# Kernel optimization log

Measured on AMD Instinct MI355X. Metric: run time of the kernel, lower is better.

Reference implementation:

```python
import jax, jax.numpy as jnp
import numpy as np

NUM_IN_CH = 64
DIM = 256
HEADS = 8


def conv1x1(x, w):
    # x: [b,c,h,w], w: [o,c,1,1] -> [b,o,h,w]
    return jnp.einsum('bchw,oc->bohw', x, w[:, :, 0, 0])


def dwconv3(x, w):
    # depthwise 3x3, padding=1; w: [c,1,3,3]
    return jax.lax.conv_general_dilated(
        x, w, window_strides=(1, 1), padding='SAME',
        feature_group_count=x.shape[1],
        dimension_numbers=('NCHW', 'OIHW', 'NCHW'))


def setup_inputs() -> dict:
    key = jax.random.key(0)
    ks = jax.random.split(key, 12)
    B, C, H, W = 8, NUM_IN_CH, 128, 128
    s = 0.02
    return {
        'x': jax.random.normal(ks[0], (B, C, H, W), jnp.float32),
        'y': jax.random.normal(ks[1], (B, C, H, W), jnp.float32),
        'z': jax.random.normal(ks[2], (B, C, H, W), jnp.float32),
        'Wq': jax.random.normal(ks[3], (DIM, C, 1, 1), jnp.float32) * s,
        'Wq_dw': jax.random.normal(ks[4], (DIM, 1, 3, 3), jnp.float32) * s,
        'Wk': jax.random.normal(ks[5], (DIM, C, 1, 1), jnp.float32) * s,
        'Wk_dw': jax.random.normal(ks[6], (DIM, 1, 3, 3), jnp.float32) * s,
        'Wv': jax.random.normal(ks[7], (DIM, C, 1, 1), jnp.float32) * s,
        'Wv_dw': jax.random.normal(ks[8], (DIM, 1, 3, 3), jnp.float32) * s,
        'Wproj': jax.random.normal(ks[9], (DIM, DIM, 1, 1), jnp.float32) * s,
        'Wfus': jax.random.normal(ks[10], (DIM, 3 * C, 1, 1), jnp.float32) * s,
        'temperature': jnp.ones((HEADS, 1, 1), jnp.float32),
    }


def reference(x, y, z, Wq, Wq_dw, Wk, Wk_dw, Wv, Wv_dw, Wproj, Wfus, temperature):
    b, c, h, w = x.shape
    hw = h * w
    q = dwconv3(conv1x1(x, Wq), Wq_dw)
    k = dwconv3(conv1x1(y, Wk), Wk_dw)
    v = dwconv3(conv1x1(z, Wv), Wv_dw)
    f = conv1x1(jnp.concatenate([x, y, z], axis=1), Wfus)

    def to_heads(t):  # [b, dim, h, w] -> [b, head, c_head, hw]
        return t.reshape(b, HEADS, DIM // HEADS, hw)

    q, k, v = to_heads(q), to_heads(k), to_heads(v)
    # L2-normalize over the spatial (hw) axis, eps matches torch F.normalize
    qn = q / jnp.maximum(jnp.sqrt(jnp.sum(q * q, axis=-1, keepdims=True)), 1e-12)
    kn = k / jnp.maximum(jnp.sqrt(jnp.sum(k * k, axis=-1, keepdims=True)), 1e-12)
    attn = jnp.einsum('bhcn,bhdn->bhcd', qn, kn) * temperature  # [b,head,c,c]
    attn = jax.nn.softmax(attn, axis=-1)
    out = jnp.einsum('bhcd,bhdn->bhcn', attn, v).reshape(b, DIM, h, w)
    out = conv1x1(out, Wproj)
    return out + f
```

## Files before the change

### kernel.cpp

```cpp
#include <hip/hip_runtime.h>
#include <cstdint>

#define B_   8
#define CIN  64
#define DIM_ 256
#define H_   128
#define W_   128
#define HW_  (H_*W_)

typedef unsigned short u16;
typedef unsigned int   u32;
typedef short short8 __attribute__((ext_vector_type(8)));
typedef float f32x4  __attribute__((ext_vector_type(4)));

__device__ __forceinline__ u16 f2bf(float f) {
    u32 u = __float_as_uint(f);
    u32 r = (u + 0x7fffu + ((u >> 16) & 1u)) >> 16;
    return (u16)r;
}
__device__ __forceinline__ float bf2f(u16 h) {
    return __uint_as_float(((u32)h) << 16);
}

__global__ __launch_bounds__(512) void convdw_kernel(
    const float* __restrict__ in, const float* __restrict__ Wc,
    const float* __restrict__ Wd, u16* __restrict__ dst)
{
    __shared__ u16 Wt[256 * 64];
    __shared__ u16 Xt[336 * 64];
    __shared__ u16 Pt[64 * 340];
    __shared__ float wlds[9 * 68];

    const int tid = threadIdx.x;
    const int tile = blockIdx.x;
    const int b = blockIdx.y;
    const int y0 = (tile >> 3) * 16;
    const int x0 = (tile & 7) * 16;

    {
        const int row = tid >> 1, hh = tid & 1;
        const float* wp = Wc + (size_t)row * 64 + hh * 32;
        #pragma unroll
        for (int s = 0; s < 4; ++s) {
            float4 f0 = *(const float4*)(wp + s * 8);
            float4 f1 = *(const float4*)(wp + s * 8 + 4);
            uint4 pk;
            pk.x = f2bf(f0.x) | ((u32)f2bf(f0.y) << 16);
            pk.y = f2bf(f0.z) | ((u32)f2bf(f0.w) << 16);
            pk.z = f2bf(f1.x) | ((u32)f2bf(f1.y) << 16);
            pk.w = f2bf(f1.z) | ((u32)f2bf(f1.w) << 16);
            int o = hh * 32 + s * 8;
            *(uint4*)&Wt[row * 64 + (o ^ ((row & 7) << 3))] = pk;
        }
    }
    {
        const float* inb = in + (size_t)b * CIN * HW_;
        for (int i = tid; i < 2592; i += 512) {
            int chg = i / 324;
            int px = i - chg * 324;
            int py = px / 18;
            int pxi = px - py * 18;
            int gy = y0 - 1 + py, gx = x0 - 1 + pxi;
            uint4 pk = make_uint4(0, 0, 0, 0);
            if (gy >= 0 && gy < H_ && gx >= 0 && gx < W_) {
                const float* sp = inb + (size_t)(chg * 8) * HW_ + (size_t)gy * W_ + gx;
                u32 wv[4];
                #pragma unroll
                for (int j = 0; j < 4; ++j) {
                    float a = sp[(size_t)(2 * j) * HW_];
                    float c = sp[(size_t)(2 * j + 1) * HW_];
                    wv[j] = f2bf(a) | ((u32)f2bf(c) << 16);
                }
                pk = make_uint4(wv[0], wv[1], wv[2], wv[3]);
            }
            *(uint4*)&Xt[px * 64 + ((chg * 8) ^ ((px & 7) << 3))] = pk;
        }
    }
    __syncthreads();

    const int lane = tid & 63, w = tid >> 6;
    const int g = lane >> 4, ln = lane & 15;
    const int wm = w & 3;
    const int wpar = w >> 2;

    u16* db = dst + (size_t)b * DIM_ * HW_;

    for (int c = 0; c < 4; ++c) {
        f32x4 acc[11];
        #pragma unroll
        for (int jj = 0; jj < 11; ++jj) acc[jj] = (f32x4){0.f, 0.f, 0.f, 0.f};
        short8 af[2];
        {
            int m = c * 64 + wm * 16 + ln;
            af[0] = *(const short8*)&Wt[m * 64 + ((g * 8) ^ ((m & 7) << 3))];
            af[1] = *(const short8*)&Wt[m * 64 + ((32 + g * 8) ^ ((m & 7) << 3))];
        }
        #pragma unroll
        for (int jj = 0; jj < 11; ++jj) {
            int j = jj * 2 + wpar;
            if (j < 21) {
                int px = j * 16 + ln;
                #pragma unroll
                for (int ks = 0; ks < 2; ++ks) {
                    short8 bf = *(const short8*)&Xt[px * 64 + ((ks * 32 + g * 8) ^ ((px & 7) << 3))];
                    acc[jj] = __builtin_amdgcn_mfma_f32_16x16x32_bf16(af[ks], bf, acc[jj], 0, 0, 0);
                }
            }
        }

        if (c > 0) __syncthreads();

        #pragma unroll
        for (int jj = 0; jj < 11; ++jj) {
            int j = jj * 2 + wpar;
            if (j < 21) {
                int px = j * 16 + ln;
                #pragma unroll
                for (int r = 0; r < 4; ++r)
                    Pt[(wm * 16 + g * 4 + r) * 340 + px] = f2bf(acc[jj][r]);
            }
        }
        for (int i = tid; i < 576; i += 512) {
            int ch = i / 9, tap = i - ch * 9;
            wlds[tap * 68 + ch] = Wd[(size_t)(c * 64 + ch) * 9 + tap];
        }
        __syncthreads();

        #pragma unroll
        for (int round = 0; round < 2; ++round) {
            int item = tid + round * 512;
            int chl = item >> 4, ox = item & 15;
            float w00 = wlds[0 * 68 + chl], w01 = wlds[1 * 68 + chl], w02 = wlds[2 * 68 + chl];
            float w10 = wlds[3 * 68 + chl], w11 = wlds[4 * 68 + chl], w12 = wlds[5 * 68 + chl];
            float w20 = wlds[6 * 68 + chl], w21 = wlds[7 * 68 + chl], w22 = wlds[8 * 68 + chl];
            const u16* prow = &Pt[chl * 340];
            u16* op = db + (size_t)(c * 64 + chl) * HW_ + x0 + ox;
            float h0m2 = 0.f, h0m1 = 0.f, h1m1 = 0.f;
            #pragma unroll
            for (int hy = 0; hy < 18; ++hy) {
                float v0 = bf2f(prow[hy * 18 + ox]);
                float v1 = bf2f(prow[hy * 18 + ox + 1]);
                float v2 = bf2f(prow[hy * 18 + ox + 2]);
                float h0 = fmaf(v0, w00, fmaf(v1, w01, v2 * w02));
                float h1 = fmaf(v0, w10, fmaf(v1, w11, v2 * w12));
                float h2 = fmaf(v0, w20, fmaf(v1, w21, v2 * w22));
                if (hy >= 2)
                    op[(size_t)(y0 + hy - 2) * W_] = f2bf(h0m2 + h1m1 + h2);
                h0m2 = h0m1; h0m1 = h0; h1m1 = h1;
            }
        }
        if (c == 3) break;
        __syncthreads();
    }
}

__global__ __launch_bounds__(256) void gram_mfma_kernel(
    const u16* __restrict__ q, const u16* __restrict__ k,
    float* __restrict__ pgram, float* __restrict__ pssq, float* __restrict__ pssk)
{
    __shared__ float red[4][1024];
    __shared__ float redq[4][32];
    __shared__ float redk[4][32];

    const int bh = blockIdx.y;
    const int chunk = blockIdx.x;
    const int tid = threadIdx.x;
    const int lane = tid & 63, wid = tid >> 6;
    const int g = lane >> 4, ln = lane & 15;

    const size_t off = (size_t)(bh * 32 + ln) * HW_ + chunk * 2048 + wid * 512 + g * 8;
    const u16* qp = q + off;
    const u16* kp = k + off;

    f32x4 aqk[2][2] = {};
    f32x4 aqq[2] = {};
    f32x4 akk[2] = {};

    #pragma unroll 4
    for (int n = 0; n < 512; n += 32) {
        short8 qf[2], kf[2];
        qf[0] = *(const short8*)(qp + n);
        qf[1] = *(const short8*)(qp + (size_t)16 * HW_ + n);
        kf[0] = *(const short8*)(kp + n);
        kf[1] = *(const short8*)(kp + (size_t)16 * HW_ + n);
        #pragma unroll
        for (int ti = 0; ti < 2; ++ti)
            #pragma unroll
            for (int tj = 0; tj < 2; ++tj)
                aqk[ti][tj] = __builtin_amdgcn_mfma_f32_16x16x32_bf16(qf[ti], kf[tj], aqk[ti][tj], 0, 0, 0);
        #pragma unroll
        for (int ti = 0; ti < 2; ++ti) {
            aqq[ti] = __builtin_amdgcn_mfma_f32_16x16x32_bf16(qf[ti], qf[ti], aqq[ti], 0, 0, 0);
            akk[ti] = __builtin_amdgcn_mfma_f32_16x16x32_bf16(kf[ti], kf[ti], akk[ti], 0, 0, 0);
        }
    }

    #pragma unroll
    for (int ti = 0; ti < 2; ++ti)
        #pragma unroll
        for (int tj = 0; tj < 2; ++tj)
            #pragma unroll
            for (int r = 0; r < 4; ++r)
                red[wid][(ti * 16 + g * 4 + r) * 32 + tj * 16 + ln] = aqk[ti][tj][r];
    if ((ln >> 2) == g) {
        #pragma unroll
        for (int ti = 0; ti < 2; ++ti) {
            redq[wid][ti * 16 + ln] = aqq[ti][ln & 3];
            redk[wid][ti * 16 + ln] = akk[ti][ln & 3];
        }
    }
    __syncthreads();

    for (int p = tid; p < 1024; p += 256) {
        float s = red[0][p] + red[1][p] + red[2][p] + red[3][p];
        pgram[((size_t)bh * 8 + chunk) * 1024 + p] = s;
    }
    if (tid < 32) {
        pssq[((size_t)bh * 8 + chunk) * 32 + tid] =
            redq[0][tid] + redq[1][tid] + redq[2][tid] + redq[3][tid];
    } else if (tid < 64) {
        int j = tid & 31;
        pssk[((size_t)bh * 8 + chunk) * 32 + j] =
            redk[0][j] + redk[1][j] + redk[2][j] + redk[3][j];
    }
}

__global__ __launch_bounds__(256) void softproj_kernel(
    const float* __restrict__ pgram, const float* __restrict__ pssq,
    const float* __restrict__ pssk, const float* __restrict__ Wproj,
    const float* __restrict__ temp, u16* __restrict__ Amm)
{
    __shared__ float att[32][33];
    __shared__ float nq[32], nk[32];

    const int bh = blockIdx.x;
    const int h = bh & 7;
    const int b = bh >> 3;
    const int tid = threadIdx.x;

    for (int p = tid; p < 1024; p += 256) {
        float s = 0.f;
        #pragma unroll
        for (int c = 0; c < 8; ++c) s += pgram[((size_t)bh * 8 + c) * 1024 + p];
        att[p >> 5][p & 31] = s;
    }
    if (tid < 32) {
        float s = 0.f;
        #pragma unroll
        for (int c = 0; c < 8; ++c) s += pssq[((size_t)bh * 8 + c) * 32 + tid];
        nq[tid] = fmaxf(sqrtf(s), 1e-12f);
    } else if (tid < 64) {
        int i = tid & 31;
        float s = 0.f;
        #pragma unroll
        for (int c = 0; c < 8; ++c) s += pssk[((size_t)bh * 8 + c) * 32 + i];
        nk[i] = fmaxf(sqrtf(s), 1e-12f);
    }
    __syncthreads();

    const float T = temp[h];
    if (tid < 32) {
        int i = tid;
        float row[32];
        float mx = -1e30f;
        float qi = T / nq[i];
        #pragma unroll
        for (int j = 0; j < 32; ++j) {
            float v = att[i][j] * qi / nk[j];
            row[j] = v;
            mx = fmaxf(mx, v);
        }
        float s = 0.f;
        #pragma unroll
        for (int j = 0; j < 32; ++j) { float e = expf(row[j] - mx); row[j] = e; s += e; }
        float inv = 1.f / s;
        #pragma unroll
        for (int j = 0; j < 32; ++j) att[i][j] = row[j] * inv;
    }
    __syncthreads();

    const int o = tid;
    float wp[32];
    #pragma unroll
    for (int i2 = 0; i2 < 32; i2 += 4)
        *(float4*)&wp[i2] = *(const float4*)&Wproj[(size_t)o * DIM_ + h * 32 + i2];
    u16* arow = Amm + ((size_t)b * DIM_ + o) * DIM_ + h * 32;
    #pragma unroll
    for (int j = 0; j < 32; ++j) {
        float s = 0.f;
        #pragma unroll
        for (int i = 0; i < 32; ++i) s = fmaf(wp[i], att[i][j], s);
        arow[j] = f2bf(s);
    }
}

__global__ __launch_bounds__(256) void wfus_cast_kernel(
    const float* __restrict__ Wfus, u16* __restrict__ Afus)
{
    int idx = blockIdx.x * 256 + threadIdx.x;
    int base = idx * 8;
    float4 f0 = *(const float4*)(Wfus + base);
    float4 f1 = *(const float4*)(Wfus + base + 4);
    uint4 pk;
    pk.x = f2bf(f0.x) | ((u32)f2bf(f0.y) << 16);
    pk.y = f2bf(f0.z) | ((u32)f2bf(f0.w) << 16);
    pk.z = f2bf(f1.x) | ((u32)f2bf(f1.y) << 16);
    pk.w = f2bf(f1.z) | ((u32)f2bf(f1.w) << 16);
    *(uint4*)(Afus + base) = pk;
}

#define LOADB_F4(KC, W) do {                                                    \
    if ((KC) < 4) {                                                             \
        _Pragma("unroll") for (int i_ = 0; i_ < 2; ++i_) {                      \
            const u16* vb_ = vbuf + ((size_t)b * DIM_ + (KC) * 64 + (qq0 + 2 * i_) * 16) * HW_ + px0 + pxu; \
            _Pragma("unroll") for (int jj_ = 0; jj_ < 8; ++jj_)                 \
                W[i_][jj_] = (u32)vb_[(size_t)(2 * jj_) * HW_]                  \
                           | ((u32)vb_[(size_t)(2 * jj_ + 1) * HW_] << 16);     \
        }                                                                       \
    } else {                                                                    \
        const float* bp_ = ((KC) == 4) ? xin : ((KC) == 5) ? yin : zin;         \
        _Pragma("unroll") for (int i_ = 0; i_ < 2; ++i_) {                      \
            const float* sp_ = bp_ + ((size_t)b * CIN + (qq0 + 2 * i_) * 16) * HW_ + px0 + pxu; \
            _Pragma("unroll") for (int jj_ = 0; jj_ < 8; ++jj_)                 \
                W[i_][jj_] = (u32)f2bf(sp_[(size_t)(2 * jj_) * HW_])            \
                           | ((u32)f2bf(sp_[(size_t)(2 * jj_ + 1) * HW_]) << 16); \
        }                                                                       \
    } } while (0)

#define WRITEB_F4(BUF, W) do {                                                  \
    u16* dd_ = &Bl[BUF][pxu * 64];                                              \
    _Pragma("unroll") for (int i_ = 0; i_ < 2; ++i_) {                          \
        int qq_ = qq0 + 2 * i_;                                                 \
        *(uint4*)&dd_[(qq_ * 16)     ^ ((pxu & 7) << 3)] = make_uint4(W[i_][0], W[i_][1], W[i_][2], W[i_][3]); \
        *(uint4*)&dd_[(qq_ * 16 + 8) ^ ((pxu & 7) << 3)] = make_uint4(W[i_][4], W[i_][5], W[i_][6], W[i_][7]); \
    } } while (0)

#define LOADA_F4(KC, A) do {                                                    \
    _Pragma("unroll") for (int ks_ = 0; ks_ < 2; ++ks_)                         \
    _Pragma("unroll") for (int fm_ = 0; fm_ < 2; ++fm_) {                       \
        int m_ = m0 + fm_ * 16 + ln;                                            \
        const u16* ap_ = ((KC) < 4)                                             \
            ? Amm + ((size_t)b * DIM_ + m_) * DIM_ + (KC) * 64 + ks_ * 32 + g * 8 \
            : Afus + (size_t)m_ * 192 + ((KC) - 4) * 64 + ks_ * 32 + g * 8;     \
        A[ks_ * 2 + fm_] = *(const short8*)ap_;                                 \
    } } while (0)

__global__ __launch_bounds__(256, 4) void final4_kernel(
    const u16* __restrict__ Amm, const u16* __restrict__ Afus,
    const u16* __restrict__ vbuf,
    const float* __restrict__ xin, const float* __restrict__ yin,
    const float* __restrict__ zin, float* __restrict__ out)
{
    __shared__ u16 Bl[2][128 * 64];

    const int tid = threadIdx.x;
    const int px0 = blockIdx.x * 128;
    const int o0  = blockIdx.y * 128;
    const int b   = blockIdx.z;
    const int lane = tid & 63, wid = tid >> 6;
    const int g = lane >> 4, ln = lane & 15;
    const int m0 = o0 + wid * 32;
    const int pxu = tid & 127;
    const int qq0 = tid >> 7;

    f32x4 acc[2][8] = {};
    short8 aC[4], aN[4];
    u32 wN[2][8];

    LOADA_F4(0, aC);
    {
        u32 w0[2][8];
        LOADB_F4(0, w0);
        WRITEB_F4(0, w0);
    }
    __syncthreads();
    LOADA_F4(1, aN);
    LOADB_F4(1, wN);

    #pragma unroll
    for (int kc = 0; kc < 7; ++kc) {
        const int cur = kc & 1;

        #pragma unroll
        for (int ks = 0; ks < 2; ++ks)
            #pragma unroll
            for (int fn = 0; fn < 8; ++fn) {
                int p = fn * 16 + ln;
                short8 bf = *(const short8*)&Bl[cur][p * 64 + ((ks * 32 + g * 8) ^ ((p & 7) << 3))];
                acc[0][fn] = __builtin_amdgcn_mfma_f32_16x16x32_bf16(aC[ks * 2 + 0], bf, acc[0][fn], 0, 0, 0);
                acc[1][fn] = __builtin_amdgcn_mfma_f32_16x16x32_bf16(aC[ks * 2 + 1], bf, acc[1][fn], 0, 0, 0);
            }

        if (kc < 6) {
            WRITEB_F4(cur ^ 1, wN);
            __syncthreads();
            #pragma unroll
            for (int r = 0; r < 4; ++r) aC[r] = aN[r];
            if (kc < 5) {
                LOADA_F4(kc + 2, aN);
                LOADB_F4(kc + 2, wN);
            }
        }
    }

    float* op = out + (size_t)b * DIM_ * HW_;
    #pragma unroll
    for (int fm = 0; fm < 2; ++fm)
        #pragma unroll
        for (int fn = 0; fn < 8; ++fn)
            #pragma unroll
            for (int r = 0; r < 4; ++r) {
                int ch = m0 + fm * 16 + g * 4 + r;
                op[(size_t)ch * HW_ + px0 + fn * 16 + ln] = acc[fm][fn][r];
            }
}

extern "C" void kernel_launch(void* const* d_in, const int* in_sizes, int n_in,
                              void* d_out, int out_size, void* d_ws, size_t ws_size,
                              hipStream_t stream) {
    (void)in_sizes; (void)n_in; (void)out_size; (void)ws_size;

    const float* x     = (const float*)d_in[0];
    const float* y     = (const float*)d_in[1];
    const float* z     = (const float*)d_in[2];
    const float* Wq    = (const float*)d_in[3];
    const float* Wqd   = (const float*)d_in[4];
    const float* Wk    = (const float*)d_in[5];
    const float* Wkd   = (const float*)d_in[6];
    const float* Wv    = (const float*)d_in[7];
    const float* Wvd   = (const float*)d_in[8];
    const float* Wproj = (const float*)d_in[9];
    const float* Wfus  = (const float*)d_in[10];
    const float* temp  = (const float*)d_in[11];

    const size_t QELEMS = (size_t)B_ * DIM_ * HW_;

    u16* qbuf = (u16*)d_out + QELEMS;
    u16* kvbuf = (u16*)d_ws;
    char* wsp = (char*)d_ws + QELEMS * sizeof(u16);
    float* pgram = (float*)wsp;                       wsp += 64 * 8 * 1024 * 4;
    float* pssq  = (float*)wsp;                       wsp += 64 * 8 * 32 * 4;
    float* pssk  = (float*)wsp;                       wsp += 64 * 8 * 32 * 4;
    u16*   Amm   = (u16*)wsp;                         wsp += (size_t)B_ * DIM_ * DIM_ * 2;
    u16*   Afus  = (u16*)wsp;

    dim3 fgrid(64, B_);

    wfus_cast_kernel<<<24, 256, 0, stream>>>(Wfus, Afus);
    convdw_kernel<<<fgrid, 512, 0, stream>>>(x, Wq, Wqd, qbuf);
    convdw_kernel<<<fgrid, 512, 0, stream>>>(y, Wk, Wkd, kvbuf);
    gram_mfma_kernel<<<dim3(8, 64), 256, 0, stream>>>(qbuf, kvbuf, pgram, pssq, pssk);
    softproj_kernel<<<64, 256, 0, stream>>>(pgram, pssq, pssk, Wproj, temp, Amm);
    convdw_kernel<<<fgrid, 512, 0, stream>>>(z, Wv, Wvd, kvbuf);
    final4_kernel<<<dim3(128, 2, B_), 256, 0, stream>>>(Amm, Afus, kvbuf, x, y, z, (float*)d_out);
}
```

Before: 277.5 us.

## Shrink convdw LDS footprint with 32-channel chunks and double-buffered weights

```diff
diff --git a/kernel.cpp b/kernel.cpp
--- a/kernel.cpp
+++ b/kernel.cpp
@@ -26,10 +26,10 @@
     const float* __restrict__ in, const float* __restrict__ Wc,
     const float* __restrict__ Wd, u16* __restrict__ dst)
 {
-    __shared__ u16 Wt[256 * 64];
+    __shared__ u16 Wtc[2][32 * 64];
     __shared__ u16 Xt[336 * 64];
-    __shared__ u16 Pt[64 * 340];
-    __shared__ float wlds[9 * 68];
+    __shared__ u16 Pt[32 * 340];
+    __shared__ float wlds[9 * 36];
 
     const int tid = threadIdx.x;
     const int tile = blockIdx.x;
@@ -38,20 +38,12 @@
     const int x0 = (tile & 7) * 16;
 
     {
-        const int row = tid >> 1, hh = tid & 1;
-        const float* wp = Wc + (size_t)row * 64 + hh * 32;
-        #pragma unroll
-        for (int s = 0; s < 4; ++s) {
-            float4 f0 = *(const float4*)(wp + s * 8);
-            float4 f1 = *(const float4*)(wp + s * 8 + 4);
-            uint4 pk;
-            pk.x = f2bf(f0.x) | ((u32)f2bf(f0.y) << 16);
-            pk.y = f2bf(f0.z) | ((u32)f2bf(f0.w) << 16);
-            pk.z = f2bf(f1.x) | ((u32)f2bf(f1.y) << 16);
-            pk.w = f2bf(f1.z) | ((u32)f2bf(f1.w) << 16);
-            int o = hh * 32 + s * 8;
-            *(uint4*)&Wt[row * 64 + (o ^ ((row & 7) << 3))] = pk;
-        }
+        const int row = tid >> 4, seg = tid & 15;
+        float4 f = *(const float4*)(Wc + (size_t)row * 64 + seg * 4);
+        uint2 pk;
+        pk.x = f2bf(f.x) | ((u32)f2bf(f.y) << 16);
+        pk.y = f2bf(f.z) | ((u32)f2bf(f.w) << 16);
+        *(uint2*)&Wtc[0][row * 64 + ((seg * 4) ^ ((row & 7) << 3))] = pk;
     }
     {
         const float* inb = in + (size_t)b * CIN * HW_;
@@ -80,24 +72,25 @@
 
     const int lane = tid & 63, w = tid >> 6;
     const int g = lane >> 4, ln = lane & 15;
-    const int wm = w & 3;
-    const int wpar = w >> 2;
+    const int wm = w & 1;
+    const int wpar = w >> 1;
 
     u16* db = dst + (size_t)b * DIM_ * HW_;
 
-    for (int c = 0; c < 4; ++c) {
-        f32x4 acc[11];
-        #pragma unroll
-        for (int jj = 0; jj < 11; ++jj) acc[jj] = (f32x4){0.f, 0.f, 0.f, 0.f};
+    for (int c = 0; c < 8; ++c) {
+        const int cb = c & 1;
+        f32x4 acc[6];
+        #pragma unroll
+        for (int jj = 0; jj < 6; ++jj) acc[jj] = (f32x4){0.f, 0.f, 0.f, 0.f};
         short8 af[2];
         {
-            int m = c * 64 + wm * 16 + ln;
-            af[0] = *(const short8*)&Wt[m * 64 + ((g * 8) ^ ((m & 7) << 3))];
-            af[1] = *(const short8*)&Wt[m * 64 + ((32 + g * 8) ^ ((m & 7) << 3))];
-        }
-        #pragma unroll
-        for (int jj = 0; jj < 11; ++jj) {
-            int j = jj * 2 + wpar;
+            int m = wm * 16 + ln;
+            af[0] = *(const short8*)&Wtc[cb][m * 64 + ((g * 8) ^ ((m & 7) << 3))];
+            af[1] = *(const short8*)&Wtc[cb][m * 64 + ((32 + g * 8) ^ ((m & 7) << 3))];
+        }
+        #pragma unroll
+        for (int jj = 0; jj < 6; ++jj) {
+            int j = jj * 4 + wpar;
             if (j < 21) {
                 int px = j * 16 + ln;
                 #pragma unroll
@@ -108,11 +101,18 @@
             }
         }
 
-        if (c > 0) __syncthreads();
-
-        #pragma unroll
-        for (int jj = 0; jj < 11; ++jj) {
-            int j = jj * 2 + wpar;
+        if (c < 7) {
+            const int row = tid >> 4, seg = tid & 15;
+            float4 f = *(const float4*)(Wc + (size_t)((c + 1) * 32 + row) * 64 + seg * 4);
+            uint2 pk;
+            pk.x = f2bf(f.x) | ((u32)f2bf(f.y) << 16);
+            pk.y = f2bf(f.z) | ((u32)f2bf(f.w) << 16);
+            *(uint2*)&Wtc[cb ^ 1][row * 64 + ((seg * 4) ^ ((row & 7) << 3))] = pk;
+        }
+
+        #pragma unroll
+        for (int jj = 0; jj < 6; ++jj) {
+            int j = jj * 4 + wpar;
             if (j < 21) {
                 int px = j * 16 + ln;
                 #pragma unroll
@@ -120,21 +120,19 @@
                     Pt[(wm * 16 + g * 4 + r) * 340 + px] = f2bf(acc[jj][r]);
             }
         }
-        for (int i = tid; i < 576; i += 512) {
+        for (int i = tid; i < 288; i += 512) {
             int ch = i / 9, tap = i - ch * 9;
-            wlds[tap * 68 + ch] = Wd[(size_t)(c * 64 + ch) * 9 + tap];
+            wlds[tap * 36 + ch] = Wd[(size_t)(c * 32 + ch) * 9 + tap];
         }
         __syncthreads();
 
-        #pragma unroll
-        for (int round = 0; round < 2; ++round) {
-            int item = tid + round * 512;
-            int chl = item >> 4, ox = item & 15;
-            float w00 = wlds[0 * 68 + chl], w01 = wlds[1 * 68 + chl], w02 = wlds[2 * 68 + chl];
-            float w10 = wlds[3 * 68 + chl], w11 = wlds[4 * 68 + chl], w12 = wlds[5 * 68 + chl];
-            float w20 = wlds[6 * 68 + chl], w21 = wlds[7 * 68 + chl], w22 = wlds[8 * 68 + chl];
+        {
+            const int chl = tid >> 4, ox = tid & 15;
+            float w00 = wlds[0 * 36 + chl], w01 = wlds[1 * 36 + chl], w02 = wlds[2 * 36 + chl];
+            float w10 = wlds[3 * 36 + chl], w11 = wlds[4 * 36 + chl], w12 = wlds[5 * 36 + chl];
+            float w20 = wlds[6 * 36 + chl], w21 = wlds[7 * 36 + chl], w22 = wlds[8 * 36 + chl];
             const u16* prow = &Pt[chl * 340];
-            u16* op = db + (size_t)(c * 64 + chl) * HW_ + x0 + ox;
+            u16* op = db + (size_t)(c * 32 + chl) * HW_ + x0 + ox;
             float h0m2 = 0.f, h0m1 = 0.f, h1m1 = 0.f;
             #pragma unroll
             for (int hy = 0; hy < 18; ++hy) {
@@ -149,8 +147,7 @@
                 h0m2 = h0m1; h0m1 = h0; h1m1 = h1;
             }
         }
-        if (c == 3) break;
-        __syncthreads();
+        if (c < 7) __syncthreads();
     }
 }
 
```

New measurement: 265.0 us. 1.05x faster.
